# Optimization experiments

Hardware: AMD Instinct MI355X
Metric: run time of the kernel (lower is better)

## Reference

```python
import jax, jax.numpy as jnp
import numpy as np

NUM_USER = 100000
NUM_ITEM = 50000
EMBED_DIM = 64
NUM_LAYER = 3
NUM_INTERACTIONS = 1600000  # symmetrized -> nnz = 3.2M
BATCH = 4096


def setup_inputs() -> dict:
    key = jax.random.key(0)
    k1, k2, k3, k4, k5, k6 = jax.random.split(key, 6)
    N = NUM_USER + NUM_ITEM
    user_emb = jax.random.normal(k1, (NUM_USER, EMBED_DIM), dtype=jnp.float32) / EMBED_DIM
    item_emb = jax.random.normal(k2, (NUM_ITEM, EMBED_DIM), dtype=jnp.float32) / EMBED_DIM
    # random bipartite interactions, symmetrized adjacency
    u = jax.random.randint(k3, (NUM_INTERACTIONS,), 0, NUM_USER, dtype=jnp.int32)
    i = jax.random.randint(k4, (NUM_INTERACTIONS,), 0, NUM_ITEM, dtype=jnp.int32) + NUM_USER
    adj_rows = jnp.concatenate([u, i])  # [nnz]
    adj_cols = jnp.concatenate([i, u])  # [nnz]
    # symmetric normalization D^-1/2 A D^-1/2
    deg = jax.ops.segment_sum(jnp.ones_like(adj_rows, dtype=jnp.float32), adj_rows, num_segments=N)
    deg = jnp.maximum(deg, 1.0)
    inv_sqrt = 1.0 / jnp.sqrt(deg)
    adj_vals = inv_sqrt[adj_rows] * inv_sqrt[adj_cols]
    user_ids = jax.random.randint(k5, (BATCH,), 0, NUM_USER, dtype=jnp.int32)
    item_ids = jax.random.randint(k6, (BATCH,), 0, NUM_ITEM, dtype=jnp.int32)
    return {"user_emb": user_emb, "item_emb": item_emb, "adj_vals": adj_vals,
            "adj_rows": adj_rows, "adj_cols": adj_cols,
            "user_ids": user_ids, "item_ids": item_ids}


def reference(user_emb, item_emb, adj_vals, adj_rows, adj_cols, user_ids, item_ids):
    num_user = user_emb.shape[0]
    N = num_user + item_emb.shape[0]
    x = jnp.concatenate([user_emb, item_emb], axis=0)  # [N, D]
    acc = x  # running sum == stack+mean over layers, fused
    for _ in range(NUM_LAYER):
        # SpMM: out[r] += vals * x[c]
        x = jax.ops.segment_sum(adj_vals[:, None] * x[adj_cols], adj_rows, num_segments=N)
        acc = acc + x
    emb = acc / (NUM_LAYER + 1)
    batch_user = emb[user_ids]                  # [B, D]
    batch_item = emb[num_user + item_ids]       # [B, D]
    scores = jnp.sum(batch_user * batch_item, axis=-1)  # DotProdScorer
    return scores
```

## Files before the change

kernel.cpp:

```cpp
#include <hip/hip_runtime.h>


#define DIM 64
#define PW 1024
#define TSHIFT 10
#define TMASK ((1 << TSHIFT) - 1)
#define STAGE_CAP 3328
#define TSTRIDE 40960

typedef unsigned short u16;
typedef unsigned char u8;
typedef unsigned int u32;

__device__ __forceinline__ u32 f2bf(float f) {
  u32 u = __float_as_uint(f);
  return (u + 0x7FFFu + ((u >> 16) & 1u)) >> 16;
}
__device__ __forceinline__ float bflo(u32 u) {
  return __uint_as_float(u << 16);
}
__device__ __forceinline__ float bfhi(u32 u) {
  return __uint_as_float(u & 0xFFFF0000u);
}


__global__ __launch_bounds__(256) void partition_direct(
    const int* __restrict__ rows, const int* __restrict__ cols, int nnz,
    int ewg, int T, int* __restrict__ tcur, u32* __restrict__ bucket) {
  __shared__ u32 raw[STAGE_CAP];
  __shared__ u8 rawt[STAGE_CAP];
  __shared__ u32 sorted[STAGE_CAP];
  __shared__ u8 sortedt[STAGE_CAP];
  __shared__ int cnt[256], lstart[256], cur[256], sc[256], gbase[256];
  int w = blockIdx.x, tid = threadIdx.x;
  cnt[tid] = 0;
  cur[tid] = 0;
  __syncthreads();
  int base = w * ewg;
  int end = min(base + ewg, nnz);
  int total = end - base;
  for (int e = base + tid, li = tid; e < end; e += 256, li += 256) {
    int r = rows[e];
    int c = cols[e];
    int t = r >> TSHIFT;
    raw[li] = ((u32)(r & TMASK) << 18) | (u32)c;
    rawt[li] = (u8)t;
    atomicAdd(&cnt[t], 1);
  }
  __syncthreads();
  sc[tid] = cnt[tid];
  __syncthreads();
  for (int off = 1; off < 256; off <<= 1) {
    int v = (tid >= off) ? sc[tid - off] : 0;
    __syncthreads();
    sc[tid] += v;
    __syncthreads();
  }
  lstart[tid] = sc[tid] - cnt[tid];
  if (tid < T)
    gbase[tid] = tid * TSTRIDE + atomicAdd(&tcur[tid], cnt[tid]);
  __syncthreads();
  for (int li = tid; li < total; li += 256) {
    int t = rawt[li];
    int slot = atomicAdd(&cur[t], 1);
    int d = lstart[t] + slot;
    sorted[d] = raw[li];
    sortedt[d] = (u8)t;
  }
  __syncthreads();
  for (int i = tid; i < total; i += 256) {
    int t = sortedt[i];
    bucket[(size_t)gbase[t] + (i - lstart[t])] = sorted[i];
  }
}


__global__ __launch_bounds__(256) void build_csr(
    const u32* __restrict__ bucket, const int* __restrict__ tcur, int T,
    int N, int* __restrict__ row_ptr, u32* __restrict__ csr) {
  __shared__ int tl[256];
  __shared__ int hist[1024];
  __shared__ int hsum[256];
  __shared__ int cur[256];
  int b = blockIdx.x;
  int t = b >> 2;
  int qt = b & 3;
  int tid = threadIdx.x;
  tl[tid] = (tid < T) ? tcur[tid] : 0;
  __syncthreads();
  for (int off = 1; off < 256; off <<= 1) {
    int v = (tid >= off) ? tl[tid - off] : 0;
    __syncthreads();
    tl[tid] += v;
    __syncthreads();
  }
  int tbase = (t == 0) ? 0 : tl[t - 1];
  int tlen = tl[t] - tbase;
  int bstart = t * TSTRIDE;
  hist[tid] = 0;
  hist[tid + 256] = 0;
  hist[tid + 512] = 0;
  hist[tid + 768] = 0;
  __syncthreads();
  const uint4* b4 = (const uint4*)(bucket + bstart);
  int nv = tlen >> 2;
  for (int i = tid; i < nv; i += 256) {
    uint4 e = b4[i];
    atomicAdd(&hist[e.x >> 18], 1);
    atomicAdd(&hist[e.y >> 18], 1);
    atomicAdd(&hist[e.z >> 18], 1);
    atomicAdd(&hist[e.w >> 18], 1);
  }
  for (int i = bstart + (nv << 2) + tid; i < bstart + tlen; i += 256)
    atomicAdd(&hist[bucket[i] >> 18], 1);
  __syncthreads();
  int h0 = hist[tid * 4], h1 = hist[tid * 4 + 1];
  int h2 = hist[tid * 4 + 2], h3 = hist[tid * 4 + 3];
  int lsum = h0 + h1 + h2 + h3;
  hsum[tid] = lsum;
  __syncthreads();
  for (int off = 1; off < 256; off <<= 1) {
    int v = (tid >= off) ? hsum[tid - off] : 0;
    __syncthreads();
    hsum[tid] += v;
    __syncthreads();
  }
  int excl = hsum[tid] - lsum;
  int o0 = excl + h0, o1 = o0 + h1, o2 = o1 + h2, o3 = o2 + h3;
  if (qt == 0) {
    int r = (t << TSHIFT) + tid * 4;
    if (r + 0 < N) row_ptr[r + 1] = tbase + o0;
    if (r + 1 < N) row_ptr[r + 2] = tbase + o1;
    if (r + 2 < N) row_ptr[r + 3] = tbase + o2;
    if (r + 3 < N) row_ptr[r + 4] = tbase + o3;
    if (t == 0 && tid == 0) row_ptr[0] = 0;
  }
  if ((tid >> 6) == qt) {
    int lq = (tid & 63) * 4;
    cur[lq + 0] = tbase + o0 - h0;
    cur[lq + 1] = tbase + o1 - h1;
    cur[lq + 2] = tbase + o2 - h2;
    cur[lq + 3] = tbase + o3 - h3;
  }
  __syncthreads();
  for (int i = tid; i < nv; i += 256) {
    uint4 e = b4[i];
    int lr;
    lr = e.x >> 18;
    if ((lr >> 8) == qt) csr[atomicAdd(&cur[lr & 255], 1)] = e.x & 0x3FFFFu;
    lr = e.y >> 18;
    if ((lr >> 8) == qt) csr[atomicAdd(&cur[lr & 255], 1)] = e.y & 0x3FFFFu;
    lr = e.z >> 18;
    if ((lr >> 8) == qt) csr[atomicAdd(&cur[lr & 255], 1)] = e.z & 0x3FFFFu;
    lr = e.w >> 18;
    if ((lr >> 8) == qt) csr[atomicAdd(&cur[lr & 255], 1)] = e.w & 0x3FFFFu;
  }
  for (int i = bstart + (nv << 2) + tid; i < bstart + tlen; i += 256) {
    u32 e = bucket[i];
    int lr = e >> 18;
    if ((lr >> 8) == qt) csr[atomicAdd(&cur[lr & 255], 1)] = e & 0x3FFFFu;
  }
}


__global__ __launch_bounds__(256) void make_y0(
    const float4* __restrict__ ue, const float4* __restrict__ ie, int U,
    int N, const int* __restrict__ row_ptr, uint4* __restrict__ y0b) {
  int i = blockIdx.x * 256 + threadIdx.x;
  int n8 = (N + 1) * 8;
  if (i >= n8) return;
  int row = i >> 3, q = i & 7;
  if (row == N) {
    y0b[i] = make_uint4(0, 0, 0, 0);
    return;
  }
  int deg = row_ptr[row + 1] - row_ptr[row];
  float invs = rsqrtf((float)max(deg, 1));
  const float4* src = (row < U) ? (ue + (size_t)row * 16 + q * 2)
                                : (ie + (size_t)(row - U) * 16 + q * 2);
  float4 a = src[0], b = src[1];
  uint4 o;
  o.x = f2bf(a.x * invs) | (f2bf(a.y * invs) << 16);
  o.y = f2bf(a.z * invs) | (f2bf(a.w * invs) << 16);
  o.z = f2bf(b.x * invs) | (f2bf(b.y * invs) << 16);
  o.w = f2bf(b.z * invs) | (f2bf(b.w * invs) << 16);
  y0b[i] = o;
}


#define ACC8(G)                                                              \
  s0 += bflo(G.x); s1 += bfhi(G.x);                                          \
  s2 += bflo(G.y); s3 += bfhi(G.y);                                          \
  s4 += bflo(G.z); s5 += bfhi(G.z);                                          \
  s6 += bflo(G.w); s7 += bfhi(G.w);

__global__ __launch_bounds__(256) void spmm_sum(
    const int* __restrict__ row_ptr, const u32* __restrict__ csr,
    const u16* __restrict__ yin, u16* __restrict__ yout, int n) {
  if (blockIdx.x == 0 && threadIdx.x < 8)
    ((uint4*)(yout + (size_t)n * DIM))[threadIdx.x] = make_uint4(0, 0, 0, 0);
  int row = (blockIdx.x * 256 + threadIdx.x) >> 3;
  int q8 = threadIdx.x & 7;
  if (row >= n) return;
  int start = row_ptr[row];
  int end = row_ptr[row + 1];
  float s0 = 0.f, s1 = 0.f, s2 = 0.f, s3 = 0.f;
  float s4 = 0.f, s5 = 0.f, s6 = 0.f, s7 = 0.f;
  int k = start;
  for (; k + 8 <= end; k += 8) {
    u32 c0 = csr[k],     c1 = csr[k + 1], c2 = csr[k + 2], c3 = csr[k + 3];
    u32 c4 = csr[k + 4], c5 = csr[k + 5], c6 = csr[k + 6], c7 = csr[k + 7];
    uint4 g0 = ((const uint4*)(yin + (size_t)c0 * DIM))[q8];
    uint4 g1 = ((const uint4*)(yin + (size_t)c1 * DIM))[q8];
    uint4 g2 = ((const uint4*)(yin + (size_t)c2 * DIM))[q8];
    uint4 g3 = ((const uint4*)(yin + (size_t)c3 * DIM))[q8];
    uint4 g4 = ((const uint4*)(yin + (size_t)c4 * DIM))[q8];
    uint4 g5 = ((const uint4*)(yin + (size_t)c5 * DIM))[q8];
    uint4 g6 = ((const uint4*)(yin + (size_t)c6 * DIM))[q8];
    uint4 g7 = ((const uint4*)(yin + (size_t)c7 * DIM))[q8];
    ACC8(g0) ACC8(g1) ACC8(g2) ACC8(g3) ACC8(g4) ACC8(g5) ACC8(g6) ACC8(g7)
  }
  for (; k + 4 <= end; k += 4) {
    u32 c0 = csr[k], c1 = csr[k + 1], c2 = csr[k + 2], c3 = csr[k + 3];
    uint4 g0 = ((const uint4*)(yin + (size_t)c0 * DIM))[q8];
    uint4 g1 = ((const uint4*)(yin + (size_t)c1 * DIM))[q8];
    uint4 g2 = ((const uint4*)(yin + (size_t)c2 * DIM))[q8];
    uint4 g3 = ((const uint4*)(yin + (size_t)c3 * DIM))[q8];
    ACC8(g0) ACC8(g1) ACC8(g2) ACC8(g3)
  }
  for (; k < end; ++k) {
    u32 c0 = csr[k];
    uint4 g0 = ((const uint4*)(yin + (size_t)c0 * DIM))[q8];
    ACC8(g0)
  }
  float inv = 1.0f / (float)max(end - start, 1);
  uint4 o;
  o.x = f2bf(s0 * inv) | (f2bf(s1 * inv) << 16);
  o.y = f2bf(s2 * inv) | (f2bf(s3 * inv) << 16);
  o.z = f2bf(s4 * inv) | (f2bf(s5 * inv) << 16);
  o.w = f2bf(s6 * inv) | (f2bf(s7 * inv) << 16);
  ((uint4*)(yout + (size_t)row * DIM))[q8] = o;
}


__device__ __forceinline__ void gather8(
    const int* __restrict__ row_ptr, const u32* __restrict__ csr,
    const u16* __restrict__ y, int row, int s, int q8, int n, float* o) {
  int start = row_ptr[row];
  int end = row_ptr[row + 1];
  float s0 = 0.f, s1 = 0.f, s2 = 0.f, s3 = 0.f;
  float s4 = 0.f, s5 = 0.f, s6 = 0.f, s7 = 0.f;
  for (int k = start + s; k < end; k += 16) {
    int k2 = k + 8;
    bool ok2 = k2 < end;
    u32 c0 = csr[k];
    u32 c1 = ok2 ? csr[k2] : (u32)n;
    uint4 g0 = ((const uint4*)(y + (size_t)c0 * DIM))[q8];
    uint4 g1 = ((const uint4*)(y + (size_t)c1 * DIM))[q8];
    ACC8(g0) ACC8(g1)
  }
  for (int m = 8; m <= 32; m <<= 1) {
    s0 += __shfl_xor(s0, m, 64); s1 += __shfl_xor(s1, m, 64);
    s2 += __shfl_xor(s2, m, 64); s3 += __shfl_xor(s3, m, 64);
    s4 += __shfl_xor(s4, m, 64); s5 += __shfl_xor(s5, m, 64);
    s6 += __shfl_xor(s6, m, 64); s7 += __shfl_xor(s7, m, 64);
  }
  o[0] = s0; o[1] = s1; o[2] = s2; o[3] = s3;
  o[4] = s4; o[5] = s5; o[6] = s6; o[7] = s7;
}

__global__ __launch_bounds__(256) void spmm3_score(
    const int* __restrict__ row_ptr, const u32* __restrict__ csr,
    const float* __restrict__ ue, const float* __restrict__ ie,
    const u16* __restrict__ y1b, const u16* __restrict__ y2b,
    const int* __restrict__ user_ids, const int* __restrict__ item_ids,
    int U, int N, int batch, float* __restrict__ out) {
  int w = (blockIdx.x * 256 + threadIdx.x) >> 6;
  int lane = threadIdx.x & 63;
  if (w >= batch) return;
  int s = lane >> 3;
  int q8 = lane & 7;
  int u = user_ids[w];
  int iti = item_ids[w];
  int it = iti + U;
  float gu[8], gi[8];
  gather8(row_ptr, csr, y2b, u, s, q8, N, gu);
  gather8(row_ptr, csr, y2b, it, s, q8, N, gi);
  int du = row_ptr[u + 1] - row_ptr[u];
  int di = row_ptr[it + 1] - row_ptr[it];
  float su = sqrtf((float)max(du, 1)), ru = 1.0f / su;
  float si = sqrtf((float)max(di, 1)), ri = 1.0f / si;
  const float4* pu = (const float4*)(ue + (size_t)u * DIM) + q8 * 2;
  const float4* pi = (const float4*)(ie + (size_t)iti * DIM) + q8 * 2;
  float4 a0a = pu[0], a0b = pu[1];
  float4 b0a = pi[0], b0b = pi[1];
  uint4 y1u = ((const uint4*)(y1b + (size_t)u * DIM))[q8];
  uint4 y2u = ((const uint4*)(y2b + (size_t)u * DIM))[q8];
  uint4 y1i = ((const uint4*)(y1b + (size_t)it * DIM))[q8];
  uint4 y2i = ((const uint4*)(y2b + (size_t)it * DIM))[q8];
  float a[8], b[8];
  a[0] = a0a.x + su * (bflo(y1u.x) + bflo(y2u.x)) + ru * gu[0];
  a[1] = a0a.y + su * (bfhi(y1u.x) + bfhi(y2u.x)) + ru * gu[1];
  a[2] = a0a.z + su * (bflo(y1u.y) + bflo(y2u.y)) + ru * gu[2];
  a[3] = a0a.w + su * (bfhi(y1u.y) + bfhi(y2u.y)) + ru * gu[3];
  a[4] = a0b.x + su * (bflo(y1u.z) + bflo(y2u.z)) + ru * gu[4];
  a[5] = a0b.y + su * (bfhi(y1u.z) + bfhi(y2u.z)) + ru * gu[5];
  a[6] = a0b.z + su * (bflo(y1u.w) + bflo(y2u.w)) + ru * gu[6];
  a[7] = a0b.w + su * (bfhi(y1u.w) + bfhi(y2u.w)) + ru * gu[7];
  b[0] = b0a.x + si * (bflo(y1i.x) + bflo(y2i.x)) + ri * gi[0];
  b[1] = b0a.y + si * (bfhi(y1i.x) + bfhi(y2i.x)) + ri * gi[1];
  b[2] = b0a.z + si * (bflo(y1i.y) + bflo(y2i.y)) + ri * gi[2];
  b[3] = b0a.w + si * (bfhi(y1i.y) + bfhi(y2i.y)) + ri * gi[3];
  b[4] = b0b.x + si * (bflo(y1i.z) + bflo(y2i.z)) + ri * gi[4];
  b[5] = b0b.y + si * (bfhi(y1i.z) + bfhi(y2i.z)) + ri * gi[5];
  b[6] = b0b.z + si * (bflo(y1i.w) + bflo(y2i.w)) + ri * gi[6];
  b[7] = b0b.w + si * (bfhi(y1i.w) + bfhi(y2i.w)) + ri * gi[7];
  float p = 0.f;
  for (int j = 0; j < 8; ++j) p += a[j] * b[j];
  p += __shfl_xor(p, 1, 64);
  p += __shfl_xor(p, 2, 64);
  p += __shfl_xor(p, 4, 64);
  if (lane == 0) out[w] = p * (1.0f / 16.0f);
}

extern "C" void kernel_launch(void* const* d_in, const int* in_sizes, int n_in,
                              void* d_out, int out_size, void* d_ws, size_t ws_size,
                              hipStream_t stream) {
  const float* user_emb = (const float*)d_in[0];
  const float* item_emb = (const float*)d_in[1];
  const int* adj_rows = (const int*)d_in[3];
  const int* adj_cols = (const int*)d_in[4];
  const int* user_ids = (const int*)d_in[5];
  const int* item_ids = (const int*)d_in[6];
  float* scores = (float*)d_out;

  const int U = in_sizes[0] / DIM;
  const int I = in_sizes[1] / DIM;
  const int N = U + I;
  const int nnz = in_sizes[2];
  const int B = in_sizes[5];

  const int T = (N + TMASK) >> TSHIFT;
  const int ewg = (nnz + PW - 1) / PW;

  char* p = (char*)d_ws;
  auto carve = [&](size_t bytes) {
    void* r = (void*)p;
    p += (bytes + 255) & ~(size_t)255;
    return r;
  };
  u16* y0b = (u16*)carve((size_t)(N + 1) * DIM * 2);
  u16* y1b = (u16*)carve((size_t)(N + 1) * DIM * 2);
  u16* y2b = (u16*)carve((size_t)(N + 1) * DIM * 2);
  int* row_ptr = (int*)carve((size_t)(N + 1) * 4);
  int* tcur = (int*)carve((size_t)T * 4);
  u32* bucket = (u32*)carve((size_t)(T + 1) * TSTRIDE * 4);
  u32* csr = (u32*)carve((size_t)nnz * 4);

  hipMemsetAsync(tcur, 0, (size_t)T * 4, stream);

  partition_direct<<<PW, 256, 0, stream>>>(adj_rows, adj_cols, nnz, ewg, T,
                                           tcur, bucket);

  build_csr<<<T * 4, 256, 0, stream>>>(bucket, tcur, T, N, row_ptr, csr);

  const int n8 = (N + 1) * 8;
  make_y0<<<(n8 + 255) / 256, 256, 0, stream>>>(
      (const float4*)user_emb, (const float4*)item_emb, U, N, row_ptr,
      (uint4*)y0b);

  const int sblocks = (N * 8 + 255) / 256;
  spmm_sum<<<sblocks, 256, 0, stream>>>(row_ptr, csr, y0b, y1b, N);
  spmm_sum<<<sblocks, 256, 0, stream>>>(row_ptr, csr, y1b, y2b, N);

  spmm3_score<<<(B + 3) / 4, 256, 0, stream>>>(row_ptr, csr, user_emb,
                                               item_emb, y1b, y2b, user_ids,
                                               item_ids, U, N, B, scores);
}
```

Before: 286.1 us.

## Fuse y0 scaling into CSR build and resize partition work chunks

Removes the separate make_y0 kernel. Each build_csr block now also writes the degree-scaled bf16 embeddings for its rows, using the per-row histogram it already holds in shared memory instead of re-reading row_ptr. Separately, the partition kernel now uses a fixed per-block edge count (EWG) with larger shared-memory staging, so fewer and bigger blocks are launched. In exchange, partition blocks use much more LDS, which lowers occupancy. The fused path also no longer writes the zero sentinel row N of y0b, which may matter if later kernels read that padding row.

```diff
diff --git a/kernel.cpp b/kernel.cpp
--- a/kernel.cpp
+++ b/kernel.cpp
@@ -2,10 +2,11 @@
 
 
 #define DIM 64
-#define PW 1024
+#define PW 544
+#define EWG 5888
 #define TSHIFT 10
 #define TMASK ((1 << TSHIFT) - 1)
-#define STAGE_CAP 3328
+#define STAGE_CAP 5888
 #define TSTRIDE 40960
 
 typedef unsigned short u16;
@@ -26,7 +27,7 @@
 
 __global__ __launch_bounds__(256) void partition_direct(
     const int* __restrict__ rows, const int* __restrict__ cols, int nnz,
-    int ewg, int T, int* __restrict__ tcur, u32* __restrict__ bucket) {
+    int T, int* __restrict__ tcur, u32* __restrict__ bucket) {
   __shared__ u32 raw[STAGE_CAP];
   __shared__ u8 rawt[STAGE_CAP];
   __shared__ u32 sorted[STAGE_CAP];
@@ -36,9 +37,10 @@
   cnt[tid] = 0;
   cur[tid] = 0;
   __syncthreads();
-  int base = w * ewg;
-  int end = min(base + ewg, nnz);
+  int base = w * EWG;
+  int end = min(base + EWG, nnz);
   int total = end - base;
+  if (total <= 0) return;
   for (int e = base + tid, li = tid; e < end; e += 256, li += 256) {
     int r = rows[e];
     int c = cols[e];
@@ -75,9 +77,11 @@
 }
 
 
-__global__ __launch_bounds__(256) void build_csr(
+__global__ __launch_bounds__(256) void build_csr_y0(
     const u32* __restrict__ bucket, const int* __restrict__ tcur, int T,
-    int N, int* __restrict__ row_ptr, u32* __restrict__ csr) {
+    int U, int N, const float4* __restrict__ ue, const float4* __restrict__ ie,
+    int* __restrict__ row_ptr, u32* __restrict__ csr,
+    uint4* __restrict__ y0b) {
   __shared__ int tl[256];
   __shared__ int hist[1024];
   __shared__ int hsum[256];
@@ -143,6 +147,23 @@
     cur[lq + 3] = tbase + o3 - h3;
   }
   __syncthreads();
+  for (int pass = 0; pass < 8; ++pass) {
+    int lr = qt * 256 + pass * 32 + (tid >> 3);
+    int q = tid & 7;
+    int row = (t << TSHIFT) + lr;
+    if (row < N) {
+      float invs = rsqrtf((float)max(hist[lr], 1));
+      const float4* src = (row < U) ? (ue + (size_t)row * 16 + q * 2)
+                                    : (ie + (size_t)(row - U) * 16 + q * 2);
+      float4 a = src[0], bb = src[1];
+      uint4 o;
+      o.x = f2bf(a.x * invs) | (f2bf(a.y * invs) << 16);
+      o.y = f2bf(a.z * invs) | (f2bf(a.w * invs) << 16);
+      o.z = f2bf(bb.x * invs) | (f2bf(bb.y * invs) << 16);
+      o.w = f2bf(bb.z * invs) | (f2bf(bb.w * invs) << 16);
+      y0b[(size_t)row * 8 + q] = o;
+    }
+  }
   for (int i = tid; i < nv; i += 256) {
     uint4 e = b4[i];
     int lr;
@@ -160,31 +181,6 @@
     int lr = e >> 18;
     if ((lr >> 8) == qt) csr[atomicAdd(&cur[lr & 255], 1)] = e & 0x3FFFFu;
   }
-}
-
-
-__global__ __launch_bounds__(256) void make_y0(
-    const float4* __restrict__ ue, const float4* __restrict__ ie, int U,
-    int N, const int* __restrict__ row_ptr, uint4* __restrict__ y0b) {
-  int i = blockIdx.x * 256 + threadIdx.x;
-  int n8 = (N + 1) * 8;
-  if (i >= n8) return;
-  int row = i >> 3, q = i & 7;
-  if (row == N) {
-    y0b[i] = make_uint4(0, 0, 0, 0);
-    return;
-  }
-  int deg = row_ptr[row + 1] - row_ptr[row];
-  float invs = rsqrtf((float)max(deg, 1));
-  const float4* src = (row < U) ? (ue + (size_t)row * 16 + q * 2)
-                                : (ie + (size_t)(row - U) * 16 + q * 2);
-  float4 a = src[0], b = src[1];
-  uint4 o;
-  o.x = f2bf(a.x * invs) | (f2bf(a.y * invs) << 16);
-  o.y = f2bf(a.z * invs) | (f2bf(a.w * invs) << 16);
-  o.z = f2bf(b.x * invs) | (f2bf(b.y * invs) << 16);
-  o.w = f2bf(b.z * invs) | (f2bf(b.w * invs) << 16);
-  y0b[i] = o;
 }
 
 
@@ -341,7 +337,7 @@
   const int B = in_sizes[5];
 
   const int T = (N + TMASK) >> TSHIFT;
-  const int ewg = (nnz + PW - 1) / PW;
+  const int npw = (nnz + EWG - 1) / EWG;
 
   char* p = (char*)d_ws;
   auto carve = [&](size_t bytes) {
@@ -359,15 +355,13 @@
 
   hipMemsetAsync(tcur, 0, (size_t)T * 4, stream);
 
-  partition_direct<<<PW, 256, 0, stream>>>(adj_rows, adj_cols, nnz, ewg, T,
-                                           tcur, bucket);
-
-  build_csr<<<T * 4, 256, 0, stream>>>(bucket, tcur, T, N, row_ptr, csr);
-
-  const int n8 = (N + 1) * 8;
-  make_y0<<<(n8 + 255) / 256, 256, 0, stream>>>(
-      (const float4*)user_emb, (const float4*)item_emb, U, N, row_ptr,
-      (uint4*)y0b);
+  partition_direct<<<npw, 256, 0, stream>>>(adj_rows, adj_cols, nnz, T, tcur,
+                                            bucket);
+
+  build_csr_y0<<<T * 4, 256, 0, stream>>>(bucket, tcur, T, U, N,
+                                          (const float4*)user_emb,
+                                          (const float4*)item_emb, row_ptr,
+                                          csr, (uint4*)y0b);
 
   const int sblocks = (N * 8 + 255) / 256;
   spmm_sum<<<sblocks, 256, 0, stream>>>(row_ptr, csr, y0b, y1b, N);
```

Result: no change. 285.1 us (-0.4%).
